# Performance work log

Measured on AMD Instinct MI355X. Metric: run time of the kernel, lower is better.

The kernel has to match this reference:

```python
import jax, jax.numpy as jnp
import numpy as np

H, T, D = 16, 4096, 64   # heads, total packed tokens, head_dim
NSEQ = 8                 # packed variable-length sequences

def setup_inputs() -> dict:
    key = jax.random.key(0)
    k1, k2, k3 = jax.random.split(key, 3)
    q = jax.random.normal(k1, (1, H, T, D), dtype=jnp.float32)
    k = jax.random.normal(k2, (1, H, T, D), dtype=jnp.float32)
    v = jax.random.normal(k3, (1, H, T, D), dtype=jnp.float32)
    # cu_seqlens: prefix sums of per-sequence lengths (equal 512-token segments here)
    cu_seqlens = jnp.arange(NSEQ + 1, dtype=jnp.int32) * (T // NSEQ)
    return {"q": q, "k": k, "v": v, "cu_seqlens": cu_seqlens,
            "block_q_len": 128, "block_k_len": 512}

def reference(q, k, v, cu_seqlens, block_q_len, block_k_len):
    # Faithful to source: scale = 1.0 / d**(-0.5) == sqrt(d)
    d = q.shape[-1]
    scale = 1.0 / d ** (-0.5)
    # [1,H,T,D] -> [T,H,D] packed layout (transpose(1,2).squeeze(0))
    qp = jnp.swapaxes(q, 1, 2)[0]
    kp = jnp.swapaxes(k, 1, 2)[0]
    vp = jnp.swapaxes(v, 1, 2)[0]
    t = qp.shape[0]
    # segment id of each packed token from cu_seqlens
    seg = jnp.searchsorted(cu_seqlens[1:], jnp.arange(t), side="right")
    # tokens attend only within their own sequence (causal=False, dropout=0)
    mask = seg[:, None] == seg[None, :]                      # [T,T]
    scores = jnp.einsum("qhd,khd->hqk", qp, kp) * scale      # [H,T,T]
    scores = jnp.where(mask[None, :, :], scores, -jnp.inf)
    p = jax.nn.softmax(scores, axis=-1)
    out = jnp.einsum("hqk,khd->qhd", p, vp)                  # [T,H,D]
    return out
```

## Files before the change

kernel.cpp:

```cpp
#include <hip/hip_runtime.h>
#include <hip/hip_bf16.h>
#include <stdint.h>

typedef short  bf16x8 __attribute__((ext_vector_type(8)));
typedef float  f32x4  __attribute__((ext_vector_type(4)));
typedef unsigned short u16;

#define HD 16
#define DD 64
#define BQ 128
#define BK 64

__device__ __forceinline__ u16 bf1(float a) {
  __hip_bfloat16 h = __float2bfloat16(a);
  union { __hip_bfloat16 h; u16 u; } cv; cv.h = h; return cv.u;
}
__device__ __forceinline__ uint32_t pk2(float a, float b) {
  __hip_bfloat162 h = __float22bfloat162_rn(make_float2(a, b));
  union { __hip_bfloat162 h; uint32_t u; } cv; cv.h = h; return cv.u;
}

__device__ __forceinline__ bf16x8 ldsw8(const u16* base, int row, int col) {
  int idx = (row * 64 + col) ^ ((row & 7) << 3);
  return *reinterpret_cast<const bf16x8*>(base + idx);
}
__device__ __forceinline__ bf16x8 ldsv8(const u16* base, int d, int col) {
  int idx = (d * 64 + col) ^ ((((d >> 2) ^ d) & 7) << 3);
  return *reinterpret_cast<const bf16x8*>(base + idx);
}

__global__ __launch_bounds__(256) void fa_fwd(
    const float* __restrict__ q, const float* __restrict__ k,
    const float* __restrict__ v, const int* __restrict__ cu,
    float* __restrict__ out, int T, int nseq, int nqt)
{
  __shared__ __align__(16) u16 sKhi[BK * DD];
  __shared__ __align__(16) u16 sKlo[BK * DD];
  __shared__ __align__(16) u16 sVt [DD * BK];
  __shared__ __align__(16) u16 sP  [4][16 * BK];

  const int nwg = nqt * HD;
  const int x8 = blockIdx.x & 7, mm = blockIdx.x >> 3;
  const int q8 = nwg >> 3, r8 = nwg & 7;
  const int wid = (x8 < r8 ? x8 * (q8 + 1) : r8 * (q8 + 1) + (x8 - r8) * q8) + mm;
  const int h    = wid / nqt;
  const int tile = wid - h * nqt;

  int seg = -1, row0 = 0, sbeg = 0, send = 0;
  {
    int acc = 0;
    for (int s = 0; s < nseq; ++s) {
      int b = cu[s], e = cu[s + 1];
      int nt = (e - b + BQ - 1) >> 7;
      if (seg < 0 && tile < acc + nt) {
        seg = s;
        int local = tile - acc;
        row0 = b + local * BQ; sbeg = b; send = e;
      }
      acc += nt;
    }
  }
  if (seg < 0) return;
  const int rows = min(BQ, send - row0);

  const int tid  = threadIdx.x;
  const int wv   = tid >> 6;
  const int lane = tid & 63;
  const int g    = lane >> 4;
  const int c    = lane & 15;

  const float SC = 8.0f * 1.4426950408889634f;
  bf16x8 qhi[2][2], qlo[2][2];
  #pragma unroll
  for (int u = 0; u < 2; ++u) {
    const int qrl = min(u * 64 + wv * 16 + c, rows - 1);
    const float* qp = q + ((size_t)h * T + (row0 + qrl)) * DD;
    #pragma unroll
    for (int w = 0; w < 2; ++w) {
      int d0 = w * 32 + g * 8;
      float4 a = *reinterpret_cast<const float4*>(qp + d0);
      float4 b = *reinterpret_cast<const float4*>(qp + d0 + 4);
      float f[8] = {a.x, a.y, a.z, a.w, b.x, b.y, b.z, b.w};
      #pragma unroll
      for (int i = 0; i < 8; ++i) {
        float s  = f[i] * SC;
        u16   hb = bf1(s);
        float hf = __uint_as_float(((uint32_t)hb) << 16);
        qhi[u][w][i] = (short)hb;
        qlo[u][w][i] = (short)bf1(s - hf);
      }
    }
  }

  const int kd0  = (tid & 15) * 4;
  const int kkey = tid >> 4;
  const int vdg  = tid & 15;
  const int vkb  = tid >> 4;

  f32x4 zero4 = {0.f, 0.f, 0.f, 0.f};
  f32x4 oacc[2][4];
  float mrun[2][4], lrun[2][4];
  #pragma unroll
  for (int u = 0; u < 2; ++u) {
    #pragma unroll
    for (int dt = 0; dt < 4; ++dt) oacc[u][dt] = zero4;
    #pragma unroll
    for (int j = 0; j < 4; ++j) { mrun[u][j] = -1e30f; lrun[u][j] = 0.f; }
  }

  const int nt = (send - sbeg + BK - 1) >> 6;

  for (int t = 0; t < nt; ++t) {
    const int kt0 = sbeg + t * BK;
    __syncthreads();

    {
      #pragma unroll
      for (int p = 0; p < 4; ++p) {
        int key = p * 16 + kkey;
        int gk  = kt0 + key; gk = gk < send ? gk : send - 1;
        float4 kv = *reinterpret_cast<const float4*>(k + ((size_t)h * T + gk) * DD + kd0);
        uint32_t h01 = pk2(kv.x, kv.y), h23 = pk2(kv.z, kv.w);
        float hf0 = __uint_as_float(h01 << 16);
        float hf1 = __uint_as_float(h01 & 0xffff0000u);
        float hf2 = __uint_as_float(h23 << 16);
        float hf3 = __uint_as_float(h23 & 0xffff0000u);
        uint32_t l01 = pk2(kv.x - hf0, kv.y - hf1), l23 = pk2(kv.z - hf2, kv.w - hf3);
        int idx = (key * 64 + kd0) ^ ((key & 7) << 3);
        uint2 hh = {h01, h23}, ll = {l01, l23};
        *reinterpret_cast<uint2*>(sKhi + idx) = hh;
        *reinterpret_cast<uint2*>(sKlo + idx) = ll;
      }
      #pragma unroll
      for (int it = 0; it < 2; ++it) {
        int kp = it * 16 + vkb;
        int g0 = kt0 + 2 * kp;     g0 = g0 < send ? g0 : send - 1;
        int g1 = kt0 + 2 * kp + 1; g1 = g1 < send ? g1 : send - 1;
        float4 va = *reinterpret_cast<const float4*>(v + ((size_t)h * T + g0) * DD + 4 * vdg);
        float4 vb = *reinterpret_cast<const float4*>(v + ((size_t)h * T + g1) * DD + 4 * vdg);
        float a[4] = {va.x, va.y, va.z, va.w};
        float b[4] = {vb.x, vb.y, vb.z, vb.w};
        #pragma unroll
        for (int i = 0; i < 4; ++i) {
          int d   = 4 * vdg + i;
          int idx = (d * 64 + 2 * kp) ^ ((((d >> 2) ^ d) & 7) << 3);
          *reinterpret_cast<uint32_t*>(sVt + idx) = pk2(a[i], b[i]);
        }
      }
    }
    __syncthreads();

    #pragma unroll
    for (int u = 0; u < 2; ++u) {
      f32x4 sacc[4];
      #pragma unroll
      for (int kt = 0; kt < 4; ++kt) sacc[kt] = zero4;
      #pragma unroll
      for (int kt = 0; kt < 4; ++kt) {
        int krow = kt * 16 + c;
        bf16x8 kh0 = ldsw8(sKhi, krow,      g * 8);
        bf16x8 kh1 = ldsw8(sKhi, krow, 32 + g * 8);
        bf16x8 kl0 = ldsw8(sKlo, krow,      g * 8);
        bf16x8 kl1 = ldsw8(sKlo, krow, 32 + g * 8);
        sacc[kt] = __builtin_amdgcn_mfma_f32_16x16x32_bf16(qhi[u][0], kh0, sacc[kt], 0, 0, 0);
        sacc[kt] = __builtin_amdgcn_mfma_f32_16x16x32_bf16(qhi[u][1], kh1, sacc[kt], 0, 0, 0);
        sacc[kt] = __builtin_amdgcn_mfma_f32_16x16x32_bf16(qlo[u][0], kh0, sacc[kt], 0, 0, 0);
        sacc[kt] = __builtin_amdgcn_mfma_f32_16x16x32_bf16(qlo[u][1], kh1, sacc[kt], 0, 0, 0);
        sacc[kt] = __builtin_amdgcn_mfma_f32_16x16x32_bf16(qhi[u][0], kl0, sacc[kt], 0, 0, 0);
        sacc[kt] = __builtin_amdgcn_mfma_f32_16x16x32_bf16(qhi[u][1], kl1, sacc[kt], 0, 0, 0);
      }

      if (kt0 + BK > send) {
        #pragma unroll
        for (int kt = 0; kt < 4; ++kt) {
          int gk = kt0 + kt * 16 + c;
          if (gk >= send) {
            sacc[kt][0] = -3.0e38f; sacc[kt][1] = -3.0e38f;
            sacc[kt][2] = -3.0e38f; sacc[kt][3] = -3.0e38f;
          }
        }
      }

      float mrow[4];
      #pragma unroll
      for (int j = 0; j < 4; ++j)
        mrow[j] = fmaxf(fmaxf(sacc[0][j], sacc[1][j]), fmaxf(sacc[2][j], sacc[3][j]));
      #pragma unroll
      for (int off = 1; off < 16; off <<= 1)
        #pragma unroll
        for (int j = 0; j < 4; ++j)
          mrow[j] = fmaxf(mrow[j], __shfl_xor(mrow[j], off, 64));

      float alpha[4];
      #pragma unroll
      for (int j = 0; j < 4; ++j) {
        float mn = fmaxf(mrun[u][j], mrow[j]);
        alpha[j] = exp2f(mrun[u][j] - mn);
        mrun[u][j] = mn;
      }

      float lrow[4] = {0.f, 0.f, 0.f, 0.f};
      u16* pb = sP[wv];
      #pragma unroll
      for (int kt = 0; kt < 4; ++kt) {
        int key = kt * 16 + c;
        #pragma unroll
        for (int j = 0; j < 4; ++j) {
          float pv = exp2f(sacc[kt][j] - mrun[u][j]);
          lrow[j] += pv;
          int row = g * 4 + j;
          pb[(row * 64 + key) ^ ((row & 7) << 3)] = bf1(pv);
        }
      }
      #pragma unroll
      for (int off = 1; off < 16; off <<= 1)
        #pragma unroll
        for (int j = 0; j < 4; ++j)
          lrow[j] += __shfl_xor(lrow[j], off, 64);
      #pragma unroll
      for (int j = 0; j < 4; ++j) lrun[u][j] = lrun[u][j] * alpha[j] + lrow[j];
      #pragma unroll
      for (int dt = 0; dt < 4; ++dt)
        #pragma unroll
        for (int j = 0; j < 4; ++j) oacc[u][dt][j] *= alpha[j];

      bf16x8 pf0 = ldsw8(pb, c,      g * 8);
      bf16x8 pf1 = ldsw8(pb, c, 32 + g * 8);
      #pragma unroll
      for (int dt = 0; dt < 4; ++dt) {
        bf16x8 v0 = ldsv8(sVt, dt * 16 + c,      g * 8);
        bf16x8 v1 = ldsv8(sVt, dt * 16 + c, 32 + g * 8);
        oacc[u][dt] = __builtin_amdgcn_mfma_f32_16x16x32_bf16(pf0, v0, oacc[u][dt], 0, 0, 0);
        oacc[u][dt] = __builtin_amdgcn_mfma_f32_16x16x32_bf16(pf1, v1, oacc[u][dt], 0, 0, 0);
      }
    }
  }

  #pragma unroll
  for (int u = 0; u < 2; ++u) {
    float inv[4];
    #pragma unroll
    for (int j = 0; j < 4; ++j) inv[j] = 1.0f / lrun[u][j];
    #pragma unroll
    for (int dt = 0; dt < 4; ++dt) {
      #pragma unroll
      for (int j = 0; j < 4; ++j) {
        int rl = u * 64 + wv * 16 + g * 4 + j;
        if (rl < rows)
          out[((size_t)(row0 + rl) * HD + h) * DD + dt * 16 + c] = oacc[u][dt][j] * inv[j];
      }
    }
  }
}

extern "C" void kernel_launch(void* const* d_in, const int* in_sizes, int n_in,
                              void* d_out, int out_size, void* d_ws, size_t ws_size,
                              hipStream_t stream) {
  const float* q  = (const float*)d_in[0];
  const float* k  = (const float*)d_in[1];
  const float* v  = (const float*)d_in[2];
  const int*   cu = (const int*)d_in[3];
  int nseq = in_sizes[3] - 1;
  int T    = in_sizes[0] / (HD * DD);
  int nqt  = T / BQ + nseq;
  int nwg  = nqt * HD;
  fa_fwd<<<dim3(nwg), dim3(256), 0, stream>>>(q, k, v, cu, (float*)d_out, T, nseq, nqt);
}
```

Baseline: 131.2 us.

## Double-buffer K/V tiles in LDS and prefetch next tile into registers

K and V shared-memory tiles become double-buffered. The global loads for the next key tile are issued into registers before the current tile's MFMA work, and converted and written to the alternate buffer afterward. This hides global load latency behind compute and drops one barrier per iteration. In exchange it doubles LDS use for K/V, which may lower occupancy, and keeps extra registers live across the compute.

```diff
diff --git a/kernel.cpp b/kernel.cpp
--- a/kernel.cpp
+++ b/kernel.cpp
@@ -34,9 +34,9 @@
     const float* __restrict__ v, const int* __restrict__ cu,
     float* __restrict__ out, int T, int nseq, int nqt)
 {
-  __shared__ __align__(16) u16 sKhi[BK * DD];
-  __shared__ __align__(16) u16 sKlo[BK * DD];
-  __shared__ __align__(16) u16 sVt [DD * BK];
+  __shared__ __align__(16) u16 sKhi[2][BK * DD];
+  __shared__ __align__(16) u16 sKlo[2][BK * DD];
+  __shared__ __align__(16) u16 sVt [2][DD * BK];
   __shared__ __align__(16) u16 sP  [4][16 * BK];
 
   const int nwg = nqt * HD;
@@ -97,6 +97,53 @@
   const int vdg  = tid & 15;
   const int vkb  = tid >> 4;
 
+  float4 kraw[4], vrawA[2], vrawB[2];
+
+  auto issue_loads = [&](int kt0) {
+    #pragma unroll
+    for (int p = 0; p < 4; ++p) {
+      int gk = kt0 + p * 16 + kkey; gk = gk < send ? gk : send - 1;
+      kraw[p] = *reinterpret_cast<const float4*>(k + ((size_t)h * T + gk) * DD + kd0);
+    }
+    #pragma unroll
+    for (int it = 0; it < 2; ++it) {
+      int kp = it * 16 + vkb;
+      int g0 = kt0 + 2 * kp;     g0 = g0 < send ? g0 : send - 1;
+      int g1 = kt0 + 2 * kp + 1; g1 = g1 < send ? g1 : send - 1;
+      vrawA[it] = *reinterpret_cast<const float4*>(v + ((size_t)h * T + g0) * DD + 4 * vdg);
+      vrawB[it] = *reinterpret_cast<const float4*>(v + ((size_t)h * T + g1) * DD + 4 * vdg);
+    }
+  };
+  auto cvt_write = [&](int b) {
+    #pragma unroll
+    for (int p = 0; p < 4; ++p) {
+      int key = p * 16 + kkey;
+      uint32_t h01 = pk2(kraw[p].x, kraw[p].y), h23 = pk2(kraw[p].z, kraw[p].w);
+      float hf0 = __uint_as_float(h01 << 16);
+      float hf1 = __uint_as_float(h01 & 0xffff0000u);
+      float hf2 = __uint_as_float(h23 << 16);
+      float hf3 = __uint_as_float(h23 & 0xffff0000u);
+      uint32_t l01 = pk2(kraw[p].x - hf0, kraw[p].y - hf1);
+      uint32_t l23 = pk2(kraw[p].z - hf2, kraw[p].w - hf3);
+      int idx = (key * 64 + kd0) ^ ((key & 7) << 3);
+      uint2 hh = {h01, h23}, ll = {l01, l23};
+      *reinterpret_cast<uint2*>(&sKhi[b][0] + idx) = hh;
+      *reinterpret_cast<uint2*>(&sKlo[b][0] + idx) = ll;
+    }
+    #pragma unroll
+    for (int it = 0; it < 2; ++it) {
+      int kp = it * 16 + vkb;
+      float a[4] = {vrawA[it].x, vrawA[it].y, vrawA[it].z, vrawA[it].w};
+      float bb[4] = {vrawB[it].x, vrawB[it].y, vrawB[it].z, vrawB[it].w};
+      #pragma unroll
+      for (int i = 0; i < 4; ++i) {
+        int d   = 4 * vdg + i;
+        int idx = (d * 64 + 2 * kp) ^ ((((d >> 2) ^ d) & 7) << 3);
+        *reinterpret_cast<uint32_t*>(&sVt[b][0] + idx) = pk2(a[i], bb[i]);
+      }
+    }
+  };
+
   f32x4 zero4 = {0.f, 0.f, 0.f, 0.f};
   f32x4 oacc[2][4];
   float mrun[2][4], lrun[2][4];
@@ -110,45 +157,19 @@
 
   const int nt = (send - sbeg + BK - 1) >> 6;
 
+  issue_loads(sbeg);
+  cvt_write(0);
+  int cur = 0;
+
   for (int t = 0; t < nt; ++t) {
     const int kt0 = sbeg + t * BK;
     __syncthreads();
-
-    {
-      #pragma unroll
-      for (int p = 0; p < 4; ++p) {
-        int key = p * 16 + kkey;
-        int gk  = kt0 + key; gk = gk < send ? gk : send - 1;
-        float4 kv = *reinterpret_cast<const float4*>(k + ((size_t)h * T + gk) * DD + kd0);
-        uint32_t h01 = pk2(kv.x, kv.y), h23 = pk2(kv.z, kv.w);
-        float hf0 = __uint_as_float(h01 << 16);
-        float hf1 = __uint_as_float(h01 & 0xffff0000u);
-        float hf2 = __uint_as_float(h23 << 16);
-        float hf3 = __uint_as_float(h23 & 0xffff0000u);
-        uint32_t l01 = pk2(kv.x - hf0, kv.y - hf1), l23 = pk2(kv.z - hf2, kv.w - hf3);
-        int idx = (key * 64 + kd0) ^ ((key & 7) << 3);
-        uint2 hh = {h01, h23}, ll = {l01, l23};
-        *reinterpret_cast<uint2*>(sKhi + idx) = hh;
-        *reinterpret_cast<uint2*>(sKlo + idx) = ll;
-      }
-      #pragma unroll
-      for (int it = 0; it < 2; ++it) {
-        int kp = it * 16 + vkb;
-        int g0 = kt0 + 2 * kp;     g0 = g0 < send ? g0 : send - 1;
-        int g1 = kt0 + 2 * kp + 1; g1 = g1 < send ? g1 : send - 1;
-        float4 va = *reinterpret_cast<const float4*>(v + ((size_t)h * T + g0) * DD + 4 * vdg);
-        float4 vb = *reinterpret_cast<const float4*>(v + ((size_t)h * T + g1) * DD + 4 * vdg);
-        float a[4] = {va.x, va.y, va.z, va.w};
-        float b[4] = {vb.x, vb.y, vb.z, vb.w};
-        #pragma unroll
-        for (int i = 0; i < 4; ++i) {
-          int d   = 4 * vdg + i;
-          int idx = (d * 64 + 2 * kp) ^ ((((d >> 2) ^ d) & 7) << 3);
-          *reinterpret_cast<uint32_t*>(sVt + idx) = pk2(a[i], b[i]);
-        }
-      }
-    }
-    __syncthreads();
+    const bool pre = (t + 1 < nt);
+    if (pre) issue_loads(kt0 + BK);
+
+    const u16* kh = sKhi[cur];
+    const u16* kl = sKlo[cur];
+    const u16* vt = sVt[cur];
 
     #pragma unroll
     for (int u = 0; u < 2; ++u) {
@@ -158,10 +179,10 @@
       #pragma unroll
       for (int kt = 0; kt < 4; ++kt) {
         int krow = kt * 16 + c;
-        bf16x8 kh0 = ldsw8(sKhi, krow,      g * 8);
-        bf16x8 kh1 = ldsw8(sKhi, krow, 32 + g * 8);
-        bf16x8 kl0 = ldsw8(sKlo, krow,      g * 8);
-        bf16x8 kl1 = ldsw8(sKlo, krow, 32 + g * 8);
+        bf16x8 kh0 = ldsw8(kh, krow,      g * 8);
+        bf16x8 kh1 = ldsw8(kh, krow, 32 + g * 8);
+        bf16x8 kl0 = ldsw8(kl, krow,      g * 8);
+        bf16x8 kl1 = ldsw8(kl, krow, 32 + g * 8);
         sacc[kt] = __builtin_amdgcn_mfma_f32_16x16x32_bf16(qhi[u][0], kh0, sacc[kt], 0, 0, 0);
         sacc[kt] = __builtin_amdgcn_mfma_f32_16x16x32_bf16(qhi[u][1], kh1, sacc[kt], 0, 0, 0);
         sacc[kt] = __builtin_amdgcn_mfma_f32_16x16x32_bf16(qlo[u][0], kh0, sacc[kt], 0, 0, 0);
@@ -228,12 +249,15 @@
       bf16x8 pf1 = ldsw8(pb, c, 32 + g * 8);
       #pragma unroll
       for (int dt = 0; dt < 4; ++dt) {
-        bf16x8 v0 = ldsv8(sVt, dt * 16 + c,      g * 8);
-        bf16x8 v1 = ldsv8(sVt, dt * 16 + c, 32 + g * 8);
+        bf16x8 v0 = ldsv8(vt, dt * 16 + c,      g * 8);
+        bf16x8 v1 = ldsv8(vt, dt * 16 + c, 32 + g * 8);
         oacc[u][dt] = __builtin_amdgcn_mfma_f32_16x16x32_bf16(pf0, v0, oacc[u][dt], 0, 0, 0);
         oacc[u][dt] = __builtin_amdgcn_mfma_f32_16x16x32_bf16(pf1, v1, oacc[u][dt], 0, 0, 0);
       }
     }
+
+    if (pre) cvt_write(cur ^ 1);
+    cur ^= 1;
   }
 
   #pragma unroll
```

New measurement: 152.6 us. 16.4% more time.

## Prefetch next K/V tile into registers while computing current tile

Applied to the files above, without the earlier changes.

Splits the K/V staging into a global-load phase and a convert-and-write-to-LDS phase. Loads for the next tile are issued into registers right after the LDS barrier, so their latency overlaps the MFMA compute of the current tile. The cost is extra registers held across the compute loop (8 float4s per thread), which may lower occupancy.

```diff
diff --git a/kernel.cpp b/kernel.cpp
--- a/kernel.cpp
+++ b/kernel.cpp
@@ -97,6 +97,53 @@
   const int vdg  = tid & 15;
   const int vkb  = tid >> 4;
 
+  float4 kraw[4], vrawA[2], vrawB[2];
+
+  auto issue_loads = [&](int kt0) {
+    #pragma unroll
+    for (int p = 0; p < 4; ++p) {
+      int gk = kt0 + p * 16 + kkey; gk = gk < send ? gk : send - 1;
+      kraw[p] = *reinterpret_cast<const float4*>(k + ((size_t)h * T + gk) * DD + kd0);
+    }
+    #pragma unroll
+    for (int it = 0; it < 2; ++it) {
+      int kp = it * 16 + vkb;
+      int g0 = kt0 + 2 * kp;     g0 = g0 < send ? g0 : send - 1;
+      int g1 = kt0 + 2 * kp + 1; g1 = g1 < send ? g1 : send - 1;
+      vrawA[it] = *reinterpret_cast<const float4*>(v + ((size_t)h * T + g0) * DD + 4 * vdg);
+      vrawB[it] = *reinterpret_cast<const float4*>(v + ((size_t)h * T + g1) * DD + 4 * vdg);
+    }
+  };
+  auto cvt_write = [&]() {
+    #pragma unroll
+    for (int p = 0; p < 4; ++p) {
+      int key = p * 16 + kkey;
+      uint32_t h01 = pk2(kraw[p].x, kraw[p].y), h23 = pk2(kraw[p].z, kraw[p].w);
+      float hf0 = __uint_as_float(h01 << 16);
+      float hf1 = __uint_as_float(h01 & 0xffff0000u);
+      float hf2 = __uint_as_float(h23 << 16);
+      float hf3 = __uint_as_float(h23 & 0xffff0000u);
+      uint32_t l01 = pk2(kraw[p].x - hf0, kraw[p].y - hf1);
+      uint32_t l23 = pk2(kraw[p].z - hf2, kraw[p].w - hf3);
+      int idx = (key * 64 + kd0) ^ ((key & 7) << 3);
+      uint2 hh = {h01, h23}, ll = {l01, l23};
+      *reinterpret_cast<uint2*>(sKhi + idx) = hh;
+      *reinterpret_cast<uint2*>(sKlo + idx) = ll;
+    }
+    #pragma unroll
+    for (int it = 0; it < 2; ++it) {
+      int kp = it * 16 + vkb;
+      float a[4] = {vrawA[it].x, vrawA[it].y, vrawA[it].z, vrawA[it].w};
+      float bb[4] = {vrawB[it].x, vrawB[it].y, vrawB[it].z, vrawB[it].w};
+      #pragma unroll
+      for (int i = 0; i < 4; ++i) {
+        int d   = 4 * vdg + i;
+        int idx = (d * 64 + 2 * kp) ^ ((((d >> 2) ^ d) & 7) << 3);
+        *reinterpret_cast<uint32_t*>(sVt + idx) = pk2(a[i], bb[i]);
+      }
+    }
+  };
+
   f32x4 zero4 = {0.f, 0.f, 0.f, 0.f};
   f32x4 oacc[2][4];
   float mrun[2][4], lrun[2][4];
@@ -110,45 +157,14 @@
 
   const int nt = (send - sbeg + BK - 1) >> 6;
 
+  issue_loads(sbeg);
+
   for (int t = 0; t < nt; ++t) {
     const int kt0 = sbeg + t * BK;
     __syncthreads();
-
-    {
-      #pragma unroll
-      for (int p = 0; p < 4; ++p) {
-        int key = p * 16 + kkey;
-        int gk  = kt0 + key; gk = gk < send ? gk : send - 1;
-        float4 kv = *reinterpret_cast<const float4*>(k + ((size_t)h * T + gk) * DD + kd0);
-        uint32_t h01 = pk2(kv.x, kv.y), h23 = pk2(kv.z, kv.w);
-        float hf0 = __uint_as_float(h01 << 16);
-        float hf1 = __uint_as_float(h01 & 0xffff0000u);
-        float hf2 = __uint_as_float(h23 << 16);
-        float hf3 = __uint_as_float(h23 & 0xffff0000u);
-        uint32_t l01 = pk2(kv.x - hf0, kv.y - hf1), l23 = pk2(kv.z - hf2, kv.w - hf3);
-        int idx = (key * 64 + kd0) ^ ((key & 7) << 3);
-        uint2 hh = {h01, h23}, ll = {l01, l23};
-        *reinterpret_cast<uint2*>(sKhi + idx) = hh;
-        *reinterpret_cast<uint2*>(sKlo + idx) = ll;
-      }
-      #pragma unroll
-      for (int it = 0; it < 2; ++it) {
-        int kp = it * 16 + vkb;
-        int g0 = kt0 + 2 * kp;     g0 = g0 < send ? g0 : send - 1;
-        int g1 = kt0 + 2 * kp + 1; g1 = g1 < send ? g1 : send - 1;
-        float4 va = *reinterpret_cast<const float4*>(v + ((size_t)h * T + g0) * DD + 4 * vdg);
-        float4 vb = *reinterpret_cast<const float4*>(v + ((size_t)h * T + g1) * DD + 4 * vdg);
-        float a[4] = {va.x, va.y, va.z, va.w};
-        float b[4] = {vb.x, vb.y, vb.z, vb.w};
-        #pragma unroll
-        for (int i = 0; i < 4; ++i) {
-          int d   = 4 * vdg + i;
-          int idx = (d * 64 + 2 * kp) ^ ((((d >> 2) ^ d) & 7) << 3);
-          *reinterpret_cast<uint32_t*>(sVt + idx) = pk2(a[i], b[i]);
-        }
-      }
-    }
+    cvt_write();
     __syncthreads();
+    if (t + 1 < nt) issue_loads(kt0 + BK);
 
     #pragma unroll
     for (int u = 0; u < 2; ++u) {
```

Measured after the change: 131.1 us. No clear change (-0.0%).
